# Performance work log

Measured on AMD Instinct MI355X. Metric: run time of the kernel, lower is better.

## Reference

```python
import jax, jax.numpy as jnp
import numpy as np

SPATIAL_SCALE = 0.25
N, C, H, W = 8, 256, 128, 128
P = 100000
IMG = 512.0  # image-space extent (H / spatial_scale)


def setup_inputs() -> dict:
    key = jax.random.key(0)
    k1, k2, k3, k4 = jax.random.split(key, 4)
    features = jax.random.normal(k1, (N, C, H, W), dtype=jnp.float32)
    batch_idx = jax.random.randint(k2, (P,), 0, N).astype(jnp.float32)
    xy = jax.random.uniform(k3, (P, 2), dtype=jnp.float32) * IMG
    rois = jnp.concatenate([batch_idx[:, None], xy], axis=1)  # [P,3]: (b, x, y)
    return {"features": features, "rois": rois}


def _interp(features, rois, spatial_scale):
    n, c, h, w = features.shape
    b = rois[:, 0].astype(jnp.int32)
    x = rois[:, 1] * spatial_scale
    y = rois[:, 2] * spatial_scale
    # RoIAlign-style bilinear interpolation with boundary handling
    valid = (y >= -1.0) & (y <= h) & (x >= -1.0) & (x <= w)
    y = jnp.maximum(y, 0.0)
    x = jnp.maximum(x, 0.0)
    y_low = jnp.floor(y).astype(jnp.int32)
    x_low = jnp.floor(x).astype(jnp.int32)
    y_at_edge = y_low >= h - 1
    x_at_edge = x_low >= w - 1
    y_low = jnp.minimum(y_low, h - 1)
    x_low = jnp.minimum(x_low, w - 1)
    y_high = jnp.where(y_at_edge, y_low, y_low + 1)
    x_high = jnp.where(x_at_edge, x_low, x_low + 1)
    y = jnp.where(y_at_edge, y_low.astype(y.dtype), y)
    x = jnp.where(x_at_edge, x_low.astype(x.dtype), x)
    ly = y - y_low
    lx = x - x_low
    hy = 1.0 - ly
    hx = 1.0 - lx
    w1 = (hy * hx)[:, None]  # [P,1]
    w2 = (hy * lx)[:, None]
    w3 = (ly * hx)[:, None]
    w4 = (ly * lx)[:, None]
    # fancy-index gather: [P, C] per corner
    v1 = features[b, :, y_low, x_low]
    v2 = features[b, :, y_low, x_high]
    v3 = features[b, :, y_high, x_low]
    v4 = features[b, :, y_high, x_high]
    out = w1 * v1 + w2 * v2 + w3 * v3 + w4 * v4  # [P, C]
    return jnp.where(valid[:, None], out, 0.0)


def reference(features, rois):
    return _interp(features, rois, SPATIAL_SCALE)
```

## Files before the change

kernel.cpp:

```cpp
#include <hip/hip_runtime.h>

#define SCALE   0.25f
#define NBATCH  8
#define CCH     256
#define HH      128
#define WW      128
#define NBUCK   (NBATCH * HH)
#define CG      32
#define NCG     (CCH / CG)
#define CAP     160
#define PADC    257
#define BIN_PASS 4


__global__ __launch_bounds__(1024) void k_bin(
    const float* __restrict__ rois, int* __restrict__ cnt,
    int4* __restrict__ slots, int P)
{
    __shared__ int lhist[NBUCK];
    __shared__ int lbase[NBUCK];
    const int t = threadIdx.x;
    lhist[t] = 0;
    __syncthreads();

    int  mybk[BIN_PASS], mypos[BIN_PASS];
    int4 myrec[BIN_PASS];
#pragma unroll
    for (int s = 0; s < BIN_PASS; ++s) {
        int p = (blockIdx.x * BIN_PASS + s) * 1024 + t;
        mybk[s] = -1;
        if (p < P) {
            float fb = rois[3 * p];
            float fx = rois[3 * p + 1] * SCALE;
            float fy = rois[3 * p + 2] * SCALE;
            int b = (int)fb;
            bool valid = (fy >= -1.0f) && (fy <= (float)HH) &&
                         (fx >= -1.0f) && (fx <= (float)WW);
            float y = fmaxf(fy, 0.0f);
            float x = fmaxf(fx, 0.0f);
            int ylo = (int)floorf(y);
            int xlo = (int)floorf(x);
            float yf = y, xf = x;
            int xhi;
            if (ylo >= HH - 1) { ylo = HH - 1; yf = (float)ylo; }
            if (xlo >= WW - 1) { xlo = WW - 1; xhi = WW - 1; xf = (float)xlo; }
            else               { xhi = xlo + 1; }
            float ly = yf - (float)ylo;
            float lx = xf - (float)xlo;
            int flo = ((xlo & 3) << 5) | (xlo >> 2);
            int fhi = ((xhi & 3) << 5) | (xhi >> 2);
            unsigned pk = (unsigned)flo | ((unsigned)fhi << 8) | (valid ? 0u : 0x80000000u);
            int bk = b * HH + ylo;
            mybk[s]  = bk;
            mypos[s] = atomicAdd(&lhist[bk], 1);
            myrec[s] = make_int4(p, (int)pk, __float_as_int(lx), __float_as_int(ly));
        }
    }
    __syncthreads();
    int h = lhist[t];
    lbase[t] = h ? atomicAdd(&cnt[t], h) : 0;
    __syncthreads();
#pragma unroll
    for (int s = 0; s < BIN_PASS; ++s) {
        int bk = mybk[s];
        if (bk >= 0) {
            int idx = lbase[bk] + mypos[s];
            if (idx < CAP) slots[bk * CAP + idx] = myrec[s];
        }
    }
}

__global__ __launch_bounds__(512, 8) void k_main(
    const float* __restrict__ feat, const int4* __restrict__ slots,
    const int* __restrict__ cnt_arr, float* __restrict__ out)
{
    const int bk = blockIdx.x & (NBUCK - 1);
    const int cg = blockIdx.x >> 10;
    const int cnt = min(cnt_arr[bk], CAP);
    if (cnt == 0) return;
    const int b  = bk >> 7;
    const int yl = bk & 127;
    const int yh = min(yl + 1, HH - 1);

    __shared__ float lds[CG * PADC];

    const int t = threadIdx.x;
    const float* base = feat + (size_t)(b * CCH + cg * CG) * (HH * WW);
#pragma unroll
    for (int k = 0; k < 4; ++k) {
        int id  = k * 512 + t;
        int x4  = id & 31;
        int row = (id >> 5) & 1;
        int c   = id >> 6;
        int y   = row ? yh : yl;
        float4 v = *(const float4*)(base + (size_t)c * (HH * WW) + y * WW + x4 * 4);
        float* d = &lds[c * PADC + row * WW + x4];
        d[0]  = v.x;
        d[32] = v.y;
        d[64] = v.z;
        d[96] = v.w;
    }
    __syncthreads();

    const int wv   = t >> 6;
    const int lane = t & 63;
    const int sub  = lane >> 4;
    const int c0   = (lane & 15) << 1;
    const float* ldc = &lds[c0 * PADC];
    const int4* sb = slots + bk * CAP;

    for (int ii = wv * 4; ii < cnt; ii += 32) {
        int i = ii + sub;
        bool act = (i < cnt);
        int4 r = sb[act ? i : cnt - 1];
        unsigned pk = (unsigned)r.y;
        float lx = __int_as_float(r.z);
        float ly = __int_as_float(r.w);
        float s  = ((int)pk < 0) ? 0.0f : 1.0f;
        float hy = (1.0f - ly) * s;
        float lys = ly * s;
        float hx = 1.0f - lx;
        float w1 = hy * hx, w2 = hy * lx, w3 = lys * hx, w4 = lys * lx;
        int flo = pk & 255;
        int fhi = (pk >> 8) & 255;

        float v1 = ldc[flo], v2 = ldc[fhi];
        float v3 = ldc[WW + flo], v4 = ldc[WW + fhi];
        float o0 = w1 * v1 + w2 * v2 + w3 * v3 + w4 * v4;
        v1 = ldc[PADC + flo]; v2 = ldc[PADC + fhi];
        v3 = ldc[PADC + WW + flo]; v4 = ldc[PADC + WW + fhi];
        float o1 = w1 * v1 + w2 * v2 + w3 * v3 + w4 * v4;

        if (act)
            *(float2*)(out + (size_t)r.x * CCH + cg * CG + c0) = make_float2(o0, o1);
    }
}

extern "C" void kernel_launch(void* const* d_in, const int* in_sizes, int n_in,
                              void* d_out, int out_size, void* d_ws, size_t ws_size,
                              hipStream_t stream) {
    const float* feat = (const float*)d_in[0];
    const float* rois = (const float*)d_in[1];
    float* out = (float*)d_out;
    const int P = in_sizes[1] / 3;

    int*  cnt   = (int*)d_ws;
    int4* slots = (int4*)((char*)d_ws + NBUCK * sizeof(int));

    hipMemsetAsync(cnt, 0, NBUCK * sizeof(int), stream);
    const int bb = (P + BIN_PASS * 1024 - 1) / (BIN_PASS * 1024);
    k_bin<<<bb, 1024, 0, stream>>>(rois, cnt, slots, P);
    k_main<<<NCG * NBUCK, 512, 0, stream>>>(feat, slots, cnt, out);
}
```

Measured before the change: 239.1 us.

## Load feature rows directly into LDS with XOR swizzle, one ROI per bin thread

The main kernel now stages the two feature rows per channel with global_load_lds straight into shared memory instead of going through registers and a padded transposed store. It uses an XOR swizzle on 16-byte chunks to avoid bank conflicts on the gather reads. The binning kernel drops its 4-ROIs-per-thread batching in favour of one ROI per thread, which launches more blocks and issues more global atomics. The swizzle math adds a few ALU ops per gather, and the direct LDS load depends on the per-lane address layout matching what the hardware writes.

```diff
diff --git a/kernel.cpp b/kernel.cpp
--- a/kernel.cpp
+++ b/kernel.cpp
@@ -9,8 +9,6 @@
 #define CG      32
 #define NCG     (CCH / CG)
 #define CAP     160
-#define PADC    257
-#define BIN_PASS 4
 
 
 __global__ __launch_bounds__(1024) void k_bin(
@@ -23,50 +21,40 @@
     lhist[t] = 0;
     __syncthreads();
 
-    int  mybk[BIN_PASS], mypos[BIN_PASS];
-    int4 myrec[BIN_PASS];
-#pragma unroll
-    for (int s = 0; s < BIN_PASS; ++s) {
-        int p = (blockIdx.x * BIN_PASS + s) * 1024 + t;
-        mybk[s] = -1;
-        if (p < P) {
-            float fb = rois[3 * p];
-            float fx = rois[3 * p + 1] * SCALE;
-            float fy = rois[3 * p + 2] * SCALE;
-            int b = (int)fb;
-            bool valid = (fy >= -1.0f) && (fy <= (float)HH) &&
-                         (fx >= -1.0f) && (fx <= (float)WW);
-            float y = fmaxf(fy, 0.0f);
-            float x = fmaxf(fx, 0.0f);
-            int ylo = (int)floorf(y);
-            int xlo = (int)floorf(x);
-            float yf = y, xf = x;
-            int xhi;
-            if (ylo >= HH - 1) { ylo = HH - 1; yf = (float)ylo; }
-            if (xlo >= WW - 1) { xlo = WW - 1; xhi = WW - 1; xf = (float)xlo; }
-            else               { xhi = xlo + 1; }
-            float ly = yf - (float)ylo;
-            float lx = xf - (float)xlo;
-            int flo = ((xlo & 3) << 5) | (xlo >> 2);
-            int fhi = ((xhi & 3) << 5) | (xhi >> 2);
-            unsigned pk = (unsigned)flo | ((unsigned)fhi << 8) | (valid ? 0u : 0x80000000u);
-            int bk = b * HH + ylo;
-            mybk[s]  = bk;
-            mypos[s] = atomicAdd(&lhist[bk], 1);
-            myrec[s] = make_int4(p, (int)pk, __float_as_int(lx), __float_as_int(ly));
-        }
+    int p = blockIdx.x * 1024 + t;
+    int mybk = -1, mypos = 0;
+    int4 myrec = make_int4(0, 0, 0, 0);
+    if (p < P) {
+        float fb = rois[3 * p];
+        float fx = rois[3 * p + 1] * SCALE;
+        float fy = rois[3 * p + 2] * SCALE;
+        int b = (int)fb;
+        bool valid = (fy >= -1.0f) && (fy <= (float)HH) &&
+                     (fx >= -1.0f) && (fx <= (float)WW);
+        float y = fmaxf(fy, 0.0f);
+        float x = fmaxf(fx, 0.0f);
+        int ylo = (int)floorf(y);
+        int xlo = (int)floorf(x);
+        float yf = y, xf = x;
+        int xhi;
+        if (ylo >= HH - 1) { ylo = HH - 1; yf = (float)ylo; }
+        if (xlo >= WW - 1) { xlo = WW - 1; xhi = WW - 1; xf = (float)xlo; }
+        else               { xhi = xlo + 1; }
+        float ly = yf - (float)ylo;
+        float lx = xf - (float)xlo;
+        unsigned pk = (unsigned)xlo | ((unsigned)xhi << 8) | (valid ? 0u : 0x80000000u);
+        int bk = b * HH + ylo;
+        mybk  = bk;
+        mypos = atomicAdd(&lhist[bk], 1);
+        myrec = make_int4(p, (int)pk, __float_as_int(lx), __float_as_int(ly));
     }
     __syncthreads();
     int h = lhist[t];
     lbase[t] = h ? atomicAdd(&cnt[t], h) : 0;
     __syncthreads();
-#pragma unroll
-    for (int s = 0; s < BIN_PASS; ++s) {
-        int bk = mybk[s];
-        if (bk >= 0) {
-            int idx = lbase[bk] + mypos[s];
-            if (idx < CAP) slots[bk * CAP + idx] = myrec[s];
-        }
+    if (mybk >= 0) {
+        int idx = lbase[mybk] + mypos;
+        if (idx < CAP) slots[mybk * CAP + idx] = myrec;
     }
 }
 
@@ -82,31 +70,35 @@
     const int yl = bk & 127;
     const int yh = min(yl + 1, HH - 1);
 
-    __shared__ float lds[CG * PADC];
+    __shared__ __align__(16) float lds[CG * 256];
 
-    const int t = threadIdx.x;
+    const int t    = threadIdx.x;
+    const int wv   = t >> 6;
+    const int lane = t & 63;
+
     const float* base = feat + (size_t)(b * CCH + cg * CG) * (HH * WW);
+    {
+        const int row = lane >> 5;
+        const int y   = row ? yh : yl;
+        const int ql  = lane & 31;
 #pragma unroll
-    for (int k = 0; k < 4; ++k) {
-        int id  = k * 512 + t;
-        int x4  = id & 31;
-        int row = (id >> 5) & 1;
-        int c   = id >> 6;
-        int y   = row ? yh : yl;
-        float4 v = *(const float4*)(base + (size_t)c * (HH * WW) + y * WW + x4 * 4);
-        float* d = &lds[c * PADC + row * WW + x4];
-        d[0]  = v.x;
-        d[32] = v.y;
-        d[64] = v.z;
-        d[96] = v.w;
+        for (int k = 0; k < 4; ++k) {
+            const int c = k * 8 + wv;
+            const int f = (c >> 1) & 7;
+            const float* g = base + (size_t)c * (HH * WW) + y * WW + ((ql ^ f) << 2);
+            __builtin_amdgcn_global_load_lds(
+                (const __attribute__((address_space(1))) unsigned int*)g,
+                (__attribute__((address_space(3))) unsigned int*)&lds[c * 256],
+                16, 0, 0);
+        }
     }
     __syncthreads();
 
-    const int wv   = t >> 6;
-    const int lane = t & 63;
-    const int sub  = lane >> 4;
-    const int c0   = (lane & 15) << 1;
-    const float* ldc = &lds[c0 * PADC];
+    const int sub = lane >> 4;
+    const int cp  = lane & 15;
+    const int c0  = cp << 1;
+    const int fc  = cp & 7;
+    const float* ldc0 = &lds[c0 * 256];
     const int4* sb = slots + bk * CAP;
 
     for (int ii = wv * 4; ii < cnt; ii += 32) {
@@ -121,14 +113,16 @@
         float lys = ly * s;
         float hx = 1.0f - lx;
         float w1 = hy * hx, w2 = hy * lx, w3 = lys * hx, w4 = lys * lx;
-        int flo = pk & 255;
-        int fhi = (pk >> 8) & 255;
+        int xlo = pk & 255;
+        int xhi = (pk >> 8) & 255;
+        int slo = (((xlo >> 2) ^ fc) << 2) | (xlo & 3);
+        int shi = (((xhi >> 2) ^ fc) << 2) | (xhi & 3);
 
-        float v1 = ldc[flo], v2 = ldc[fhi];
-        float v3 = ldc[WW + flo], v4 = ldc[WW + fhi];
+        float v1 = ldc0[slo],       v2 = ldc0[shi];
+        float v3 = ldc0[128 + slo], v4 = ldc0[128 + shi];
         float o0 = w1 * v1 + w2 * v2 + w3 * v3 + w4 * v4;
-        v1 = ldc[PADC + flo]; v2 = ldc[PADC + fhi];
-        v3 = ldc[PADC + WW + flo]; v4 = ldc[PADC + WW + fhi];
+        v1 = ldc0[256 + slo];       v2 = ldc0[256 + shi];
+        v3 = ldc0[384 + slo];       v4 = ldc0[384 + shi];
         float o1 = w1 * v1 + w2 * v2 + w3 * v3 + w4 * v4;
 
         if (act)
@@ -148,7 +142,7 @@
     int4* slots = (int4*)((char*)d_ws + NBUCK * sizeof(int));
 
     hipMemsetAsync(cnt, 0, NBUCK * sizeof(int), stream);
-    const int bb = (P + BIN_PASS * 1024 - 1) / (BIN_PASS * 1024);
+    const int bb = (P + 1023) / 1024;
     k_bin<<<bb, 1024, 0, stream>>>(rois, cnt, slots, P);
     k_main<<<NCG * NBUCK, 512, 0, stream>>>(feat, slots, cnt, out);
 }
```

Result: no change. 237.2 us (-0.8%).
